# Performance work log

Measured on AMD Instinct MI355X. Metric: run time of the kernel, lower is better.

The kernel has to match this reference:

```python
import jax, jax.numpy as jnp
import numpy as np

K = 3          # deformable conv kernel size
PAD = 1        # padding
BN_EPS = 1e-5


def _upsample2(x):
    # nn.Upsample(scale_factor=2) default mode='nearest' on [B,C,D,H,W]
    x = jnp.repeat(x, 2, axis=2)
    x = jnp.repeat(x, 2, axis=3)
    x = jnp.repeat(x, 2, axis=4)
    return x


def _conv3d(x, w, b):
    out = jax.lax.conv_general_dilated(
        x, w, window_strides=(1, 1, 1), padding=[(PAD, PAD)] * 3,
        dimension_numbers=('NCDHW', 'OIDHW', 'NCDHW'))
    return out + b[None, :, None, None, None]


def _trilinear_sample(x, coords):
    # x: [B,C,D,H,W]; coords: [B,Kt,3,D,H,W] absolute (possibly OOB) positions.
    # Zero padding outside the volume (standard deformable-conv convention).
    B, C, D, H, W = x.shape
    pd, ph, pw = coords[:, :, 0], coords[:, :, 1], coords[:, :, 2]  # [B,Kt,D,H,W]
    d0 = jnp.floor(pd); h0 = jnp.floor(ph); w0 = jnp.floor(pw)
    fd = pd - d0; fh = ph - h0; fw = pw - w0
    x_flat = x.reshape(B, C, D * H * W)

    def gather(di, hi, wi):
        valid = ((di >= 0) & (di < D) & (hi >= 0) & (hi < H) & (wi >= 0) & (wi < W))
        dc = jnp.clip(di, 0, D - 1).astype(jnp.int32)
        hc = jnp.clip(hi, 0, H - 1).astype(jnp.int32)
        wc = jnp.clip(wi, 0, W - 1).astype(jnp.int32)
        flat = (dc * H + hc) * W + wc                       # [B,Kt,D,H,W]
        vals = jax.vmap(lambda xf, idx: jnp.take(xf, idx.reshape(-1), axis=1))(x_flat, flat)
        vals = vals.reshape(B, C, *flat.shape[1:])          # [B,C,Kt,D,H,W]
        return vals * valid[:, None].astype(x.dtype)

    out = jnp.zeros((B, C) + pd.shape[1:], x.dtype)
    for dd in (0, 1):
        for hh in (0, 1):
            for ww in (0, 1):
                wgt = ((fd if dd else 1.0 - fd)
                       * (fh if hh else 1.0 - fh)
                       * (fw if ww else 1.0 - fw))           # [B,Kt,D,H,W]
                out = out + gather(d0 + dd, h0 + hh, w0 + ww) * wgt[:, None]
    return out  # [B,C,Kt,D,H,W]


def _deform_conv3d(x, w_off, b_off, w, b):
    B, C, D, H, W = x.shape
    Kt = K ** 3
    # offsets: Conv3d(C, 3*K^3, k=3, pad=1) -> [B, Kt, 3(dz,dy,dx), D,H,W]
    off = _conv3d(x, w_off, b_off).reshape(B, Kt, 3, D, H, W)
    # kernel tap displacements relative to output voxel: [Kt,3]
    taps = jnp.stack(jnp.meshgrid(jnp.arange(K), jnp.arange(K), jnp.arange(K),
                                  indexing='ij'), -1).reshape(-1, 3).astype(x.dtype) - PAD
    grid = jnp.stack(jnp.meshgrid(jnp.arange(D, dtype=x.dtype),
                                  jnp.arange(H, dtype=x.dtype),
                                  jnp.arange(W, dtype=x.dtype),
                                  indexing='ij'), 0)          # [3,D,H,W]
    coords = grid[None, None] + taps[None, :, :, None, None, None] + off  # [B,Kt,3,D,H,W]
    sampled = _trilinear_sample(x, coords)                    # [B,C,Kt,D,H,W]
    out = jnp.einsum('bckdhw,ock->bodhw', sampled, w.reshape(w.shape[0], C, Kt))
    return out + b[None, :, None, None, None]


def setup_inputs() -> dict:
    key = jax.random.key(0)
    ks = jax.random.split(key, 4)
    ch_in, ch_out = 64, 32
    x = jax.random.normal(ks[0], (1, ch_in, 16, 16, 16), jnp.float32)
    w_off = jax.random.normal(ks[1], (3 * K ** 3, ch_in, K, K, K), jnp.float32) * 0.01
    b_off = jnp.zeros((3 * K ** 3,), jnp.float32)
    w = jax.random.normal(ks[2], (ch_out, ch_in, K, K, K), jnp.float32) * 0.05
    b = jnp.zeros((ch_out,), jnp.float32)
    gamma = jnp.ones((ch_out,), jnp.float32)
    beta = jnp.zeros((ch_out,), jnp.float32)
    return {"x": x, "w_off": w_off, "b_off": b_off, "w": w, "b": b,
            "gamma": gamma, "beta": beta}


def reference(x, w_off, b_off, w, b, gamma, beta):
    x = _upsample2(x)                                  # [B,C,2D,2H,2W]
    out = _deform_conv3d(x, w_off, b_off, w, b)        # [B,ch_out,2D,2H,2W]
    # BatchNorm3d (training-mode batch stats) + ReLU
    mean = out.mean(axis=(0, 2, 3, 4), keepdims=True)
    var = out.var(axis=(0, 2, 3, 4), keepdims=True)
    out = (out - mean) * jax.lax.rsqrt(var + BN_EPS)
    out = out * gamma[None, :, None, None, None] + beta[None, :, None, None, None]
    return jax.nn.relu(out)
```

## Files before the change

### kernel.cpp

```cpp
#include <hip/hip_runtime.h>
#include <math.h>

#define NVOX  32768
#define CIN   64
#define COUT  32
#define KT    27
#define CIT   1728
#define PSP   5832

#define WS_XT   0
#define WS_WA   186624
#define WS_WO   214272
#define WS_STAT 297216

#define SST 584

typedef __attribute__((ext_vector_type(8))) _Float16 half8;
typedef __attribute__((ext_vector_type(2))) _Float16 half2v;
typedef __attribute__((ext_vector_type(4))) float floatx4;

static __device__ __forceinline__ unsigned dup16(float w) {
    unsigned short b = __builtin_bit_cast(unsigned short, (_Float16)w);
    return (unsigned)b * 0x10001u;
}
static __device__ __forceinline__ half2v u2h2(unsigned u) {
    return __builtin_bit_cast(half2v, u);
}

__global__ __launch_bounds__(256) void prep_all_kernel(
        const float* __restrict__ x, const float* __restrict__ w_off,
        const float* __restrict__ wmat, float* __restrict__ ws) {
    int b = blockIdx.x, t = threadIdx.x;
    if (b < 92) {
        __shared__ _Float16 tile[64][65];
        _Float16* xth = (_Float16*)(ws + WS_XT);
        int tq = t >> 6, lane = t & 63;
        int base = b * 64;
        int cell = base + lane;
        int qw = cell % 18, qh = (cell / 18) % 18, qd = cell / 324;
        bool interior = (cell < PSP) && qd >= 1 && qd <= 16 && qh >= 1 && qh <= 16
                        && qw >= 1 && qw <= 16;
        int xbase = interior ? (((qd - 1) * 16 + (qh - 1)) * 16 + (qw - 1)) : 0;
#pragma unroll
        for (int i = 0; i < 16; i++) {
            int c = tq * 16 + i;
            float v = interior ? x[c * 4096 + xbase] : 0.f;
            tile[lane][c] = (_Float16)v;
        }
        __syncthreads();
#pragma unroll
        for (int i = 0; i < 16; i++) {
            int s = tq * 16 + i;
            int cell2 = base + s;
            if (cell2 < PSP) xth[cell2 * 64 + lane] = tile[s][lane];
        }
    } else if (b < 119) {
        _Float16* wa = (_Float16*)(ws + WS_WA);
        int idx = (b - 92) * 256 + t;
        int kb = idx >> 5, o = idx & 31;
        half8 r;
#pragma unroll
        for (int j = 0; j < 8; j++) {
            int kk = kb * 8 + j;
            int tap = kk >> 6, ci = kk & 63;
            r[j] = (_Float16)wmat[o * CIT + ci * 27 + tap];
        }
        *(half8*)(wa + idx * 8) = r;
    } else if (b < 200) {
        _Float16* wo = (_Float16*)(ws + WS_WO);
        int idx = (b - 119) * 256 + t;
        int kb = idx / 96, m = idx % 96;
        half8 r;
#pragma unroll
        for (int j = 0; j < 8; j++) {
            int kk = kb * 8 + j;
            int tap = kk >> 6, ci = kk & 63;
            float v = (m < 81) ? w_off[(m * 64 + ci) * 27 + tap] : 0.f;
            r[j] = (_Float16)v;
        }
        *(half8*)(wo + idx * 8) = r;
    } else {
        if (t < 64) ws[WS_STAT + t] = 0.f;
    }
}

__global__ __launch_bounds__(256) void deform_kernel(
        const float* __restrict__ b_off, const float* __restrict__ bias,
        float* ws, float* __restrict__ out) {
    __shared__ __align__(16) unsigned short smem[16 * SST];
    __shared__ __align__(16) _Float16 Plh[81 * 16];
    __shared__ __align__(16) char ubuf[9216];
    __shared__ float rsum[COUT], rsq[COUT];

    float*    red  = (float*)ubuf;
    int*      cba  = (int*)ubuf;
    unsigned* cbw  = (unsigned*)(ubuf + 4608);
    float*    pbuf = (float*)ubuf;

    const half2v* xt2 = (const half2v*)(ws + WS_XT);
    const unsigned* xtu = (const unsigned*)(ws + WS_XT);
    const half8* wa8 = (const half8*)(ws + WS_WA);
    const half8* wo8 = (const half8*)(ws + WS_WO);
    float* gstat = ws + WS_STAT;

    int tid = threadIdx.x, wave = tid >> 6, lane = tid & 63;
    int vsel = lane >> 5, cl = lane & 31;
    int pbase = blockIdx.x * 16;
    int d = pbase >> 10, h = (pbase >> 5) & 31, w0 = pbase & 31;

    if (tid < COUT) { rsum[tid] = 0.f; rsq[tid] = 0.f; }

    int mh = wave & 1, kh = wave >> 1;
    int col = lane & 15, quad = lane >> 4;

    floatx4 oacc0 = {0.f,0.f,0.f,0.f}, oacc1 = {0.f,0.f,0.f,0.f}, oacc2 = {0.f,0.f,0.f,0.f};
#pragma unroll 1
    for (int g = 0; g < 3; g++) {
        if (g) __syncthreads();
        int rd = ((d + g - 1) >> 1) + 1;
#pragma unroll
        for (int tl = 0; tl < 9; tl++) {
            int kh2 = tl / 3, kw2 = tl % 3;
            int rh = ((h + kh2 - 1) >> 1) + 1;
#pragma unroll
            for (int pi = 0; pi < 2; pi++) {
                int v = wave * 4 + pi * 2 + vsel;
                int w = w0 + v;
                int rw = ((w + kw2 - 1) >> 1) + 1;
                int cell = (rd * 18 + rh) * 18 + rw;
                unsigned uv = xtu[cell * 32 + cl];
                *(unsigned*)(smem + v * SST + tl * 64 + 2 * cl) = uv;
            }
        }
        __syncthreads();
#pragma unroll
        for (int s = 0; s < 9; s++) {
            int k_local = kh * 288 + s * 32;
            int kb = ((g * 576 + k_local) >> 3) + quad;
            half8 bfrag = *(const half8*)(smem + col * SST + k_local + quad * 8);
            half8 a0 = wo8[kb * 96 + mh * 48 + col];
            half8 a1 = wo8[kb * 96 + mh * 48 + 16 + col];
            half8 a2 = wo8[kb * 96 + mh * 48 + 32 + col];
            oacc0 = __builtin_amdgcn_mfma_f32_16x16x32_f16(a0, bfrag, oacc0, 0, 0, 0);
            oacc1 = __builtin_amdgcn_mfma_f32_16x16x32_f16(a1, bfrag, oacc1, 0, 0, 0);
            oacc2 = __builtin_amdgcn_mfma_f32_16x16x32_f16(a2, bfrag, oacc2, 0, 0, 0);
        }
    }
    __syncthreads();
    if (kh == 1) {
#pragma unroll
        for (int r = 0; r < 4; r++) {
            red[(mh * 48 +      quad * 4 + r) * 16 + col] = oacc0[r];
            red[(mh * 48 + 16 + quad * 4 + r) * 16 + col] = oacc1[r];
            red[(mh * 48 + 32 + quad * 4 + r) * 16 + col] = oacc2[r];
        }
    }
    __syncthreads();
    if (kh == 0) {
#pragma unroll
        for (int r = 0; r < 4; r++) {
            int m0 = mh * 48 + quad * 4 + r;
            Plh[m0 * 16 + col] = (_Float16)(oacc0[r] + red[m0 * 16 + col] + b_off[m0]);
            int m1 = m0 + 16;
            Plh[m1 * 16 + col] = (_Float16)(oacc1[r] + red[m1 * 16 + col] + b_off[m1]);
            int m2 = m0 + 32;
            if (m2 < 81)
                Plh[m2 * 16 + col] = (_Float16)(oacc2[r] + red[m2 * 16 + col] + b_off[m2]);
        }
    }

    int mt = wave & 1;
    floatx4 acc = {0.f, 0.f, 0.f, 0.f};

#pragma unroll 1
    for (int g = 0; g < 3; g++) {
        __syncthreads();
        if (tid < 144) {
            int v = tid & 15, tl = tid >> 4;
            int tap = g * 9 + tl;
            int kh2 = tl / 3, kw2 = tl % 3;
            int w = w0 + v;
            float od = (float)Plh[(3 * tap + 0) * 16 + v];
            float oh = (float)Plh[(3 * tap + 1) * 16 + v];
            float ow = (float)Plh[(3 * tap + 2) * 16 + v];
            float pdc = (float)(d + g - 1) + od;
            float phc = (float)(h + kh2 - 1) + oh;
            float pwc = (float)(w + kw2 - 1) + ow;
            float fd0 = floorf(pdc), fh0 = floorf(phc), fw0 = floorf(pwc);
            float fd = pdc - fd0, fh = phc - fh0, fw = pwc - fw0;
            int id = (int)fd0, ih = (int)fh0, iw = (int)fw0;
            int rd0 = ((min(max(id,     -2), 33) >> 1) + 1) * (324 * 32);
            int rd1 = ((min(max(id + 1, -2), 33) >> 1) + 1) * (324 * 32);
            int rh0 = ((min(max(ih,     -2), 33) >> 1) + 1) * (18 * 32);
            int rh1 = ((min(max(ih + 1, -2), 33) >> 1) + 1) * (18 * 32);
            int rw0 = ((min(max(iw,     -2), 33) >> 1) + 1) * 32;
            int rw1 = ((min(max(iw + 1, -2), 33) >> 1) + 1) * 32;
            int* A = cba + tid * 8;
            unsigned* W = cbw + tid * 8;
            A[0] = rd0 + rh0 + rw0; A[1] = rd0 + rh0 + rw1;
            A[2] = rd0 + rh1 + rw0; A[3] = rd0 + rh1 + rw1;
            A[4] = rd1 + rh0 + rw0; A[5] = rd1 + rh0 + rw1;
            A[6] = rd1 + rh1 + rw0; A[7] = rd1 + rh1 + rw1;
            float gd = 1.f - fd, gh = 1.f - fh, gw = 1.f - fw;
            W[0] = dup16(gd * gh * gw); W[1] = dup16(gd * gh * fw);
            W[2] = dup16(gd * fh * gw); W[3] = dup16(gd * fh * fw);
            W[4] = dup16(fd * gh * gw); W[5] = dup16(fd * gh * fw);
            W[6] = dup16(fd * fh * gw); W[7] = dup16(fd * fh * fw);
        }
        __syncthreads();

#pragma unroll
        for (int tl = 0; tl < 9; tl++) {
#pragma unroll
            for (int pi = 0; pi < 2; pi++) {
                int v = wave * 4 + pi * 2 + vsel;
                int item = tl * 16 + v;
                const int4* a4 = (const int4*)(cba + item * 8);
                const int4* w4 = (const int4*)(cbw + item * 8);
                int4 A0 = a4[0], A1 = a4[1];
                int4 U0 = w4[0], U1 = w4[1];
                half2v s = u2h2(U0.x) * xt2[A0.x + cl];
                s += u2h2(U0.y) * xt2[A0.y + cl];
                s += u2h2(U0.z) * xt2[A0.z + cl];
                s += u2h2(U0.w) * xt2[A0.w + cl];
                s += u2h2(U1.x) * xt2[A1.x + cl];
                s += u2h2(U1.y) * xt2[A1.y + cl];
                s += u2h2(U1.z) * xt2[A1.z + cl];
                s += u2h2(U1.w) * xt2[A1.w + cl];
                *(unsigned*)(smem + v * SST + tl * 64 + 2 * cl) =
                    __builtin_bit_cast(unsigned, s);
            }
        }
        __syncthreads();

#pragma unroll
        for (int s = 0; s < 9; s++) {
            int k_local = kh * 288 + s * 32;
            int kb = ((g * 576 + k_local) >> 3) + quad;
            half8 afrag = wa8[kb * 32 + mt * 16 + col];
            half8 bfrag = *(const half8*)(smem + col * SST + k_local + quad * 8);
            acc = __builtin_amdgcn_mfma_f32_16x16x32_f16(afrag, bfrag, acc, 0, 0, 0);
        }
    }
    __syncthreads();

    if (kh == 1) {
#pragma unroll
        for (int r = 0; r < 4; r++) pbuf[mt * 256 + (quad * 4 + r) * 16 + col] = acc[r];
    }
    __syncthreads();
    if (kh == 0) {
#pragma unroll
        for (int r = 0; r < 4; r++) {
            int o = mt * 16 + quad * 4 + r;
            float val = acc[r] + pbuf[mt * 256 + (quad * 4 + r) * 16 + col] + bias[o];
            out[o * NVOX + pbase + col] = val;
            atomicAdd(&rsum[o], val);
            atomicAdd(&rsq[o], val * val);
        }
    }
    __syncthreads();
    if (tid < COUT) {
        atomicAdd(&gstat[tid], rsum[tid]);
        atomicAdd(&gstat[COUT + tid], rsq[tid]);
    }
}

__global__ void bn_kernel(const float* __restrict__ ws,
                          const float* __restrict__ gamma,
                          const float* __restrict__ beta,
                          float* out) {
    int i = blockIdx.x * 256 + threadIdx.x;
    int o = i >> 15;
    const float* gstat = ws + WS_STAT;
    const float inv = 1.f / 32768.f;
    float mean = gstat[o] * inv;
    float var  = gstat[COUT + o] * inv - mean * mean;
    float sc   = rsqrtf(var + 1e-5f) * gamma[o];
    float v = (out[i] - mean) * sc + beta[o];
    out[i] = fmaxf(v, 0.f);
}

extern "C" void kernel_launch(void* const* d_in, const int* in_sizes, int n_in,
                              void* d_out, int out_size, void* d_ws, size_t ws_size,
                              hipStream_t stream) {
    const float* x     = (const float*)d_in[0];
    const float* w_off = (const float*)d_in[1];
    const float* b_off = (const float*)d_in[2];
    const float* wmat  = (const float*)d_in[3];
    const float* bias  = (const float*)d_in[4];
    const float* gamma = (const float*)d_in[5];
    const float* beta  = (const float*)d_in[6];
    float* ws  = (float*)d_ws;
    float* out = (float*)d_out;

    prep_all_kernel<<<201, 256, 0, stream>>>(x, w_off, wmat, ws);
    deform_kernel<<<2048, 256, 0, stream>>>(b_off, bias, ws, out);
    bn_kernel<<<4096, 256, 0, stream>>>(ws, gamma, beta, out);
}
```

Measured before the change: 166.3 us.

## Stage deduplicated low-res input slab once and index it directly for offset conv

The offset-conv stage used to gather an im2col tile into shared memory once per kernel depth slice, with a barrier between slices. It now loads the small set of low-resolution source cells (2x2x10 cells, 32 dwords each, padded stride) into shared memory once. The MFMA B fragments are then read straight from that slab, with index arithmetic that maps each tap to its nearest-upsampled source cell. This removes duplicate global loads and two barriers, at the cost of extra integer index math and possible LDS bank conflicts from the new access pattern.

```diff
diff --git a/kernel.cpp b/kernel.cpp
--- a/kernel.cpp
+++ b/kernel.cpp
@@ -114,36 +114,48 @@
     int col = lane & 15, quad = lane >> 4;
 
     floatx4 oacc0 = {0.f,0.f,0.f,0.f}, oacc1 = {0.f,0.f,0.f,0.f}, oacc2 = {0.f,0.f,0.f,0.f};
+    {
+        int rdbase = ((d - 1) >> 1) + 1;
+        int rhbase = ((h - 1) >> 1) + 1;
+        int rwbase = ((w0 - 1) >> 1) + 1;
+        unsigned* slabu = (unsigned*)ubuf;
+        for (int i = tid; i < 1280; i += 256) {
+            int cell = i >> 5, cl2 = i & 31;
+            int rdL = cell / 20, rem = cell - rdL * 20;
+            int rhL = rem / 10, rwL = rem - rhL * 10;
+            int gc = ((rdbase + rdL) * 18 + rhbase + rhL) * 18 + rwbase + rwL;
+            slabu[cell * 36 + cl2] = xtu[gc * 32 + cl2];
+        }
+    }
+    __syncthreads();
+    {
+        const _Float16* slabh = (const _Float16*)ubuf;
+        int q8 = quad * 8;
+        int colp1 = col + 1;
+        int hadj = (h & 1) ^ 1;
+        int khb = kh * 288;
 #pragma unroll 1
-    for (int g = 0; g < 3; g++) {
-        if (g) __syncthreads();
-        int rd = ((d + g - 1) >> 1) + 1;
-#pragma unroll
-        for (int tl = 0; tl < 9; tl++) {
-            int kh2 = tl / 3, kw2 = tl % 3;
-            int rh = ((h + kh2 - 1) >> 1) + 1;
-#pragma unroll
-            for (int pi = 0; pi < 2; pi++) {
-                int v = wave * 4 + pi * 2 + vsel;
-                int w = w0 + v;
-                int rw = ((w + kw2 - 1) >> 1) + 1;
-                int cell = (rd * 18 + rh) * 18 + rw;
-                unsigned uv = xtu[cell * 32 + cl];
-                *(unsigned*)(smem + v * SST + tl * 64 + 2 * cl) = uv;
+        for (int g = 0; g < 3; g++) {
+            int rdL20 = ((g == 2) || (g == 1 && !(d & 1))) ? 20 : 0;
+#pragma unroll
+            for (int s = 0; s < 9; s++) {
+                int k = khb + s * 32 + q8;
+                int tl = k >> 6;
+                int ch0 = k & 63;
+                int kh2 = (tl * 171) >> 9;
+                int kw2 = tl - 3 * kh2;
+                int rhL = (kh2 + hadj) >> 1;
+                int rwL = (colp1 + kw2) >> 1;
+                int idx = rdL20 + rhL * 10 + rwL;
+                half8 bfrag = *(const half8*)(slabh + idx * 72 + ch0);
+                int kb = (g * 576 + k) >> 3;
+                half8 a0 = wo8[kb * 96 + mh * 48 + col];
+                half8 a1 = wo8[kb * 96 + mh * 48 + 16 + col];
+                half8 a2 = wo8[kb * 96 + mh * 48 + 32 + col];
+                oacc0 = __builtin_amdgcn_mfma_f32_16x16x32_f16(a0, bfrag, oacc0, 0, 0, 0);
+                oacc1 = __builtin_amdgcn_mfma_f32_16x16x32_f16(a1, bfrag, oacc1, 0, 0, 0);
+                oacc2 = __builtin_amdgcn_mfma_f32_16x16x32_f16(a2, bfrag, oacc2, 0, 0, 0);
             }
-        }
-        __syncthreads();
-#pragma unroll
-        for (int s = 0; s < 9; s++) {
-            int k_local = kh * 288 + s * 32;
-            int kb = ((g * 576 + k_local) >> 3) + quad;
-            half8 bfrag = *(const half8*)(smem + col * SST + k_local + quad * 8);
-            half8 a0 = wo8[kb * 96 + mh * 48 + col];
-            half8 a1 = wo8[kb * 96 + mh * 48 + 16 + col];
-            half8 a2 = wo8[kb * 96 + mh * 48 + 32 + col];
-            oacc0 = __builtin_amdgcn_mfma_f32_16x16x32_f16(a0, bfrag, oacc0, 0, 0, 0);
-            oacc1 = __builtin_amdgcn_mfma_f32_16x16x32_f16(a1, bfrag, oacc1, 0, 0, 0);
-            oacc2 = __builtin_amdgcn_mfma_f32_16x16x32_f16(a2, bfrag, oacc2, 0, 0, 0);
         }
     }
     __syncthreads();
```

After: 168.4 us. Within noise of the previous version (+1.3%).
